# Optimization experiments

Measured on AMD Instinct MI355X. Metric: run time of the kernel, lower is better.

The kernel has to match this reference:

```python
import jax, jax.numpy as jnp
import numpy as np

K = 15  # dynamic kernel size (out conv emits 15*15=225 channels)


def conv3x3(x, w, b):
    # x: [B,C,H,W], w: [O,I,3,3] (OIHW), 'SAME' padding, stride 1
    y = jax.lax.conv_general_dilated(
        x, w, window_strides=(1, 1), padding='SAME',
        dimension_numbers=('NCHW', 'OIHW', 'NCHW'))
    return y + b[None, :, None, None]


def res_block(x, wa, ba, wb, bb):
    # ResidualBlock_noBN: x + conv(relu(conv(x)))
    return x + conv3x3(jax.nn.relu(conv3x3(x, wa, ba)), wb, bb)


def setup_inputs() -> dict:
    key = jax.random.key(0)
    ks = jax.random.split(key, 12)
    nf = 64

    def w(k, o, i):
        return jax.random.normal(k, (o, i, 3, 3), jnp.float32) * 0.05

    return {
        'data_with_est': jax.random.normal(ks[0], (4, 6, 256, 256), jnp.float32),
        'data': jax.random.normal(ks[1], (4, 3, 256, 256), jnp.float32),
        'w_first': w(ks[2], nf, 6), 'b_first': jnp.zeros((nf,), jnp.float32),
        'w1a': w(ks[3], nf, nf), 'b1a': jnp.zeros((nf,), jnp.float32),
        'w1b': w(ks[4], nf, nf), 'b1b': jnp.zeros((nf,), jnp.float32),
        'w2a': w(ks[5], nf, nf), 'b2a': jnp.zeros((nf,), jnp.float32),
        'w2b': w(ks[6], nf, nf), 'b2b': jnp.zeros((nf,), jnp.float32),
        'w3a': w(ks[7], nf, nf), 'b3a': jnp.zeros((nf,), jnp.float32),
        'w3b': w(ks[8], nf, nf), 'b3b': jnp.zeros((nf,), jnp.float32),
        'w_out': w(ks[9], K * K, nf), 'b_out': jnp.zeros((K * K,), jnp.float32),
    }


def kernel_conv(frames, core):
    # frames: [B,3,H,W]; core: [B,225,H,W]
    B, C, H, W = frames.shape
    # per-pixel softmax over the 225 kernel taps of |core| (N=1, color=1 in original view)
    weights = jax.nn.softmax(jnp.abs(core), axis=1)  # [B, K*K, H, W]
    p = K // 2
    pad = jnp.pad(frames, ((0, 0), (0, 0), (p, p), (p, p)))
    shifts = jnp.arange(K)

    def win(i, j):  # shifted window, matches frame_pad[..., i:i+H, j:j+W]
        return jax.lax.dynamic_slice(pad, (0, 0, i, j), (B, C, H, W))

    # [K, K, B, C, H, W]; flattened index i*K+j matches torch stacking order
    patches = jax.vmap(lambda i: jax.vmap(lambda j: win(i, j))(shifts))(shifts)
    patches = patches.reshape(K * K, B, C, H, W)
    pred = jnp.einsum('bkhw,kbchw->bchw', weights, patches)  # sum over taps
    return pred


def reference(data_with_est, data,
              w_first, b_first,
              w1a, b1a, w1b, b1b,
              w2a, b2a, w2b, b2b,
              w3a, b3a, w3b, b3b,
              w_out, b_out):
    x = conv3x3(data_with_est, w_first, b_first)
    x = res_block(x, w1a, b1a, w1b, b1b)
    x = res_block(x, w2a, b2a, w2b, b2b)
    x = res_block(x, w3a, b3a, w3b, b3b)
    core = conv3x3(x, w_out, b_out)  # [B,225,H,W]
    pred = kernel_conv(data, core)   # [B,3,H,W]
    # original returns [frames, pred]
    return (data, pred)
```

## Files before the change

kernel.cpp:

```cpp
#include <hip/hip_runtime.h>

#define HW 256
#define PW 258
#define PP (PW * PW)
#define NPIX (HW * HW)

using short8 = __attribute__((ext_vector_type(8))) short;
using short4v = __attribute__((ext_vector_type(4))) short;
using f32x4 = __attribute__((ext_vector_type(4))) float;
using h4 = __attribute__((ext_vector_type(4))) _Float16;
using h8 = __attribute__((ext_vector_type(8))) _Float16;

#define GLD_LDS(g, l)                                                  \
  __builtin_amdgcn_global_load_lds(                                    \
      (const __attribute__((address_space(1))) void*)(g),              \
      (__attribute__((address_space(3))) void*)(l), 16, 0, 0)

static __device__ __forceinline__ ushort f2bf(float f) {
  unsigned u = __float_as_uint(f);
  unsigned r = (u + 0x7FFFu + ((u >> 16) & 1u)) >> 16;
  return (ushort)r;
}
static __device__ __forceinline__ float bf2f(ushort u) {
  return __uint_as_float(((unsigned)u) << 16);
}

__global__ void pack_in_k(const float* __restrict__ din, ushort* __restrict__ xp) {
  int i = blockIdx.x * 256 + threadIdx.x;
  int b = i >> 16;
  int px = i & 65535;
  int y = px >> 8, x = px & 255;
  short8 v;
#pragma unroll
  for (int z = 0; z < 8; ++z) v[z] = 0;
#pragma unroll
  for (int ic = 0; ic < 6; ++ic)
    v[ic] = (short)f2bf(din[(b * 6 + ic) * NPIX + px]);
  *(short8*)&xp[((size_t)b * PP + (size_t)(y + 1) * PW + (x + 1)) * 8] = v;
}

__global__ void zero_halo_k(ushort* __restrict__ x, ushort* __restrict__ y,
                            ushort* __restrict__ xp) {
  int i = blockIdx.x * 256 + threadIdx.x;
  if (i >= 4 * 1028) return;
  int b = i / 1028;
  int h = i - b * 1028;
  int py, px;
  if (h < 258) { py = 0; px = h; }
  else if (h < 516) { py = 257; px = h - 258; }
  else if (h < 772) { py = h - 516 + 1; px = 0; }
  else { py = h - 772 + 1; px = 257; }
  size_t p = (size_t)b * PP + (size_t)py * PW + px;
  short8 z;
#pragma unroll
  for (int k = 0; k < 8; ++k) z[k] = 0;
#pragma unroll
  for (int c8 = 0; c8 < 8; ++c8) {
    *(short8*)&x[p * 64 + c8 * 8] = z;
    *(short8*)&y[p * 64 + c8 * 8] = z;
  }
  *(short8*)&xp[p * 8] = z;
}

__global__ void pack_wfrag_k(const float* __restrict__ w,
                             ushort* __restrict__ wf, int OC, int CIN,
                             int CPAD, int NG, int total) {
  int i = blockIdx.x * 256 + threadIdx.x;
  if (i >= total) return;
  int j = i & 7;
  int lane = (i >> 3) & 63;
  int rest = i >> 9;
  int g = rest % NG;
  int ks = rest / NG;
  int oc = g * 16 + (lane & 15);
  int k = ks * 32 + (lane >> 4) * 8 + j;
  int t = k / CPAD;
  int ic = k - t * CPAD;
  float v = 0.f;
  if (oc < OC && t < 9 && ic < CIN) v = w[(oc * CIN + ic) * 9 + t];
  wf[i] = f2bf(v);
}

template <int C, int KS, bool RELU, bool RESID>
__global__ __launch_bounds__(256, 2) void conv_mfma_k(
    const ushort* __restrict__ in, const ushort* __restrict__ wf,
    const float* __restrict__ bias, const ushort* __restrict__ resid,
    ushort* __restrict__ out) {
  constexpr int CV = C / 8;
  constexpr int SROW = 66 * CV;
  constexpr int TOT = 6 * SROW;
  constexpr int LSLOT = ((TOT + 63) / 64) * 64;
  constexpr int W = (KS > 6) ? 6 : KS;
  __shared__ __align__(16) ushort xs[LSLOT * 8];

  const int tid = threadIdx.x;
  const int wave = tid >> 6, lane = tid & 63;
  const int quad = lane >> 4, l15 = lane & 15;
  const int x0 = blockIdx.x * 64, y0 = blockIdx.y * 4, b = blockIdx.z;
  const ushort* inb = in + (size_t)b * PP * C;
  const ushort* wfl = wf + (size_t)lane * 8;

  for (int s0 = wave * 64; s0 < TOT; s0 += 256) {
    int s = s0 + lane;
    int row, col, chunk;
    if (C == 64) {
      row = s / SROW;
      int r = s - row * SROW;
      col = r >> 3;
      chunk = (r & 7) ^ (col & 7);
    } else {
      row = s / 66;
      col = s - row * 66;
      chunk = 0;
    }
    GLD_LDS(inb + ((size_t)(y0 + row) * PW + (x0 + col)) * C + chunk * 8,
            &xs[(size_t)s0 * 8]);
  }

  short8 Wa[4][W];
  auto loadA = [&](int slot, int ks) {
#pragma unroll
    for (int mt = 0; mt < 4; ++mt)
      Wa[mt][slot] = *(const short8*)&wfl[(size_t)(ks * 4 + mt) * 512];
  };
#pragma unroll
  for (int ks = 0; ks < W; ++ks) loadA(ks, ks);

  __syncthreads();

  f32x4 acc[4][4];
#pragma unroll
  for (int mt = 0; mt < 4; ++mt)
#pragma unroll
    for (int nt = 0; nt < 4; ++nt)
#pragma unroll
      for (int r = 0; r < 4; ++r) acc[mt][nt][r] = 0.f;

  auto loadB = [&](short8* B, int ks) {
    int t, chunk;
    if (C == 64) {
      t = ks >> 1;
      chunk = ((ks & 1) << 2) + quad;
    } else {
      t = ks * 4 + quad;
      if (t > 8) t = 8;
      chunk = 0;
    }
    int dy = t / 3, dx = t - (t / 3) * 3;
#pragma unroll
    for (int nt = 0; nt < 4; ++nt) {
      int c = nt * 16 + l15 + dx;
      int slot = (C == 64)
                     ? ((wave + dy) * SROW + c * 8 + (chunk ^ (c & 7)))
                     : ((wave + dy) * 66 + c);
      B[nt] = *(const short8*)&xs[(size_t)slot * 8];
    }
  };

  short8 B0[4], B1[4];
  loadB(B0, 0);
#pragma unroll
  for (int ks = 0; ks < KS; ++ks) {
    if (ks + 1 < KS) loadB(B1, ks + 1);
    const int slot = ks % W;
#pragma unroll
    for (int nt = 0; nt < 4; ++nt)
#pragma unroll
      for (int mt = 0; mt < 4; ++mt)
        acc[mt][nt] = __builtin_amdgcn_mfma_f32_16x16x32_bf16(
            Wa[mt][slot], B0[nt], acc[mt][nt], 0, 0, 0);
    if (ks + W < KS) loadA(slot, ks + W);
#pragma unroll
    for (int nt = 0; nt < 4; ++nt) B0[nt] = B1[nt];
  }

  const int yw = y0 + wave;
#pragma unroll
  for (int mt = 0; mt < 4; ++mt) {
    const float4 bb = *(const float4*)&bias[mt * 16 + quad * 4];
#pragma unroll
    for (int nt = 0; nt < 4; ++nt) {
      int px = x0 + nt * 16 + l15;
      size_t base = ((size_t)b * PP + (size_t)(yw + 1) * PW + (px + 1)) * 64 +
                    mt * 16 + quad * 4;
      float v0 = acc[mt][nt][0] + bb.x;
      float v1 = acc[mt][nt][1] + bb.y;
      float v2 = acc[mt][nt][2] + bb.z;
      float v3 = acc[mt][nt][3] + bb.w;
      if (RELU) {
        v0 = fmaxf(v0, 0.f); v1 = fmaxf(v1, 0.f);
        v2 = fmaxf(v2, 0.f); v3 = fmaxf(v3, 0.f);
      }
      if (RESID) {
        short4v rv = *(const short4v*)&resid[base];
        v0 += bf2f((ushort)rv[0]); v1 += bf2f((ushort)rv[1]);
        v2 += bf2f((ushort)rv[2]); v3 += bf2f((ushort)rv[3]);
      }
      short4v o;
      o[0] = (short)f2bf(v0); o[1] = (short)f2bf(v1);
      o[2] = (short)f2bf(v2); o[3] = (short)f2bf(v3);
      *(short4v*)&out[base] = o;
    }
  }
}

__global__ __launch_bounds__(256, 2) void out_kc_k(
    const ushort* __restrict__ x, const ushort* __restrict__ wf,
    const float* __restrict__ b_out, const float* __restrict__ data,
    float* __restrict__ pred) {
  __shared__ __align__(16) char uni[64 * 264 * 2];
  __shared__ float dsh[3][15][78];
  __shared__ float bsh[256];
  ushort* xs = (ushort*)uni;
  _Float16* coreSh = (_Float16*)uni;

  const int tid = threadIdx.x;
  const int wave = tid >> 6, lane = tid & 63;
  const int quad = lane >> 4, l15 = lane & 15;
  const int x0 = blockIdx.x * 64, y = blockIdx.y, b = blockIdx.z;
  const ushort* wfl = wf + (size_t)lane * 8;

  for (int s0 = wave * 64; s0 < 3 * 528; s0 += 256) {
    int s = s0 + lane;
    int row = s / 528;
    int r = s - row * 528;
    int col = r >> 3;
    int chunk = (r & 7) ^ (col & 7);
    const ushort* g = x + ((size_t)b * PP + (size_t)(y + row) * PW +
                           (x0 + col)) * 64 + chunk * 8;
    GLD_LDS(g, &xs[(size_t)s0 * 8]);
  }
  bsh[tid] = (tid < 225) ? b_out[tid] : 0.f;
  for (int i = tid; i < 3 * 15 * 78; i += 256) {
    int ch = i / 1170;
    int rem = i - ch * 1170;
    int r = rem / 78;
    int cc = rem - r * 78;
    int gy = y - 7 + r, gx = x0 - 7 + cc;
    float v = 0.f;
    if ((unsigned)gy < (unsigned)HW && (unsigned)gx < (unsigned)HW)
      v = data[((b * 3 + ch) << 16) + (gy << 8) + gx];
    dsh[ch][r][cc] = v;
  }

  short8 Wa[4][6];
  auto loadA = [&](int slot, int ks) {
#pragma unroll
    for (int mt = 0; mt < 4; ++mt)
      Wa[mt][slot] =
          *(const short8*)&wfl[(size_t)((ks * 16 + wave * 4 + mt)) * 512];
  };
#pragma unroll
  for (int ks = 0; ks < 6; ++ks) loadA(ks, ks);

  __syncthreads();

  f32x4 acc[4][4];
#pragma unroll
  for (int mt = 0; mt < 4; ++mt)
#pragma unroll
    for (int nt = 0; nt < 4; ++nt)
#pragma unroll
      for (int r = 0; r < 4; ++r) acc[mt][nt][r] = 0.f;

  auto loadB = [&](short8* B, int ks) {
    int t = ks >> 1;
    int dy = t / 3, dx = t - (t / 3) * 3;
    int chunk = ((ks & 1) << 2) + quad;
#pragma unroll
    for (int nt = 0; nt < 4; ++nt) {
      int c = nt * 16 + l15 + dx;
      int slot = dy * 528 + c * 8 + (chunk ^ (c & 7));
      B[nt] = *(const short8*)&xs[(size_t)slot * 8];
    }
  };

  short8 B0[4], B1[4];
  loadB(B0, 0);
#pragma unroll
  for (int ks = 0; ks < 18; ++ks) {
    if (ks + 1 < 18) loadB(B1, ks + 1);
    const int slot = ks % 6;
#pragma unroll
    for (int nt = 0; nt < 4; ++nt)
#pragma unroll
      for (int mt = 0; mt < 4; ++mt)
        acc[mt][nt] = __builtin_amdgcn_mfma_f32_16x16x32_bf16(
            Wa[mt][slot], B0[nt], acc[mt][nt], 0, 0, 0);
    if (ks + 6 < 18) loadA(slot, ks + 6);
#pragma unroll
    for (int nt = 0; nt < 4; ++nt) B0[nt] = B1[nt];
  }
  __syncthreads();

#pragma unroll
  for (int mt = 0; mt < 4; ++mt) {
    int c0 = wave * 64 + mt * 16 + quad * 4;
#pragma unroll
    for (int nt = 0; nt < 4; ++nt) {
      int px = nt * 16 + l15;
      h4 hv;
#pragma unroll
      for (int r = 0; r < 4; ++r) {
        int c = c0 + r;
        float a = acc[mt][nt][r] + bsh[c];
        a = (c < 225) ? fabsf(a) : -1e4f;
        hv[r] = (_Float16)a;
      }
      *(h4*)&coreSh[px * 264 + c0] = hv;
    }
  }
  __syncthreads();

  const int px = wave * 16 + l15;
  const int cbase = quad * 64;
  h8 vals[8];
#pragma unroll
  for (int v = 0; v < 8; ++v)
    vals[v] = *(h8*)&coreSh[px * 264 + cbase + v * 8];

  float m = 0.f;
#pragma unroll
  for (int v = 0; v < 8; ++v)
#pragma unroll
    for (int z = 0; z < 8; ++z) m = fmaxf(m, (float)vals[v][z]);
  m = fmaxf(m, __shfl_xor(m, 16));
  m = fmaxf(m, __shfl_xor(m, 32));

  float l = 0.f, p0 = 0.f, p1 = 0.f, p2 = 0.f;
#pragma unroll
  for (int v = 0; v < 8; ++v)
#pragma unroll
    for (int z = 0; z < 8; ++z) {
      int c = cbase + v * 8 + z;
      float a = (float)vals[v][z];
      float e = __expf(a - m);
      l += e;
      if (c < 225) {
        int di = (int)(((unsigned)c * 34953u) >> 19);
        int dj = c - di * 15;
        p0 += e * dsh[0][di][px + dj];
        p1 += e * dsh[1][di][px + dj];
        p2 += e * dsh[2][di][px + dj];
      }
    }
  l += __shfl_xor(l, 16);  l += __shfl_xor(l, 32);
  p0 += __shfl_xor(p0, 16); p0 += __shfl_xor(p0, 32);
  p1 += __shfl_xor(p1, 16); p1 += __shfl_xor(p1, 32);
  p2 += __shfl_xor(p2, 16); p2 += __shfl_xor(p2, 32);

  if (quad == 0) {
    float inv = 1.f / l;
    int pix = (y << 8) + x0 + px;
    pred[((b * 3 + 0) << 16) + pix] = p0 * inv;
    pred[((b * 3 + 1) << 16) + pix] = p1 * inv;
    pred[((b * 3 + 2) << 16) + pix] = p2 * inv;
  }
}

__global__ void copy_k(const float4* __restrict__ src, float4* __restrict__ dst,
                       int n4) {
  int i = blockIdx.x * blockDim.x + threadIdx.x;
  if (i < n4) dst[i] = src[i];
}

extern "C" void kernel_launch(void* const* d_in, const int* in_sizes, int n_in,
                              void* d_out, int out_size, void* d_ws,
                              size_t ws_size, hipStream_t stream) {
  const float* data_with_est = (const float*)d_in[0];
  const float* data = (const float*)d_in[1];
  const float* w_first = (const float*)d_in[2];
  const float* b_first = (const float*)d_in[3];
  const float* wa[3] = {(const float*)d_in[4], (const float*)d_in[8],
                        (const float*)d_in[12]};
  const float* ba[3] = {(const float*)d_in[5], (const float*)d_in[9],
                        (const float*)d_in[13]};
  const float* wb[3] = {(const float*)d_in[6], (const float*)d_in[10],
                        (const float*)d_in[14]};
  const float* bb[3] = {(const float*)d_in[7], (const float*)d_in[11],
                        (const float*)d_in[15]};
  const float* w_out = (const float*)d_in[16];
  const float* b_out = (const float*)d_in[17];

  float* out = (float*)d_out;
  float* pred = out + 4 * 3 * NPIX;

  ushort* x = (ushort*)d_ws;
  ushort* y = x + (size_t)4 * PP * 64;
  ushort* xp = y + (size_t)4 * PP * 64;
  ushort* Wp1 = xp + (size_t)4 * PP * 8;
  ushort* Wpr = Wp1 + 6144;
  ushort* Wpo = Wpr + 6 * 36864;

  pack_in_k<<<1024, 256, 0, stream>>>(data_with_est, xp);
  zero_halo_k<<<17, 256, 0, stream>>>(x, y, xp);
  pack_wfrag_k<<<24, 256, 0, stream>>>(w_first, Wp1, 64, 6, 8, 4, 6144);
  for (int i = 0; i < 3; ++i) {
    pack_wfrag_k<<<144, 256, 0, stream>>>(wa[i], Wpr + (2 * i) * 36864, 64, 64,
                                          64, 4, 36864);
    pack_wfrag_k<<<144, 256, 0, stream>>>(wb[i], Wpr + (2 * i + 1) * 36864, 64,
                                          64, 64, 4, 36864);
  }
  pack_wfrag_k<<<576, 256, 0, stream>>>(w_out, Wpo, 225, 64, 64, 16, 147456);

  dim3 cgrid(4, 64, 4), cblk(256);
  conv_mfma_k<8, 3, false, false>
      <<<cgrid, cblk, 0, stream>>>(xp, Wp1, b_first, nullptr, x);
  for (int i = 0; i < 3; ++i) {
    conv_mfma_k<64, 18, true, false><<<cgrid, cblk, 0, stream>>>(
        x, Wpr + (2 * i) * 36864, ba[i], nullptr, y);
    conv_mfma_k<64, 18, false, true><<<cgrid, cblk, 0, stream>>>(
        y, Wpr + (2 * i + 1) * 36864, bb[i], x, x);
  }
  out_kc_k<<<dim3(4, HW, 4), 256, 0, stream>>>(x, Wpo, b_out, data, pred);
  int n4 = 4 * 3 * NPIX / 4;
  copy_k<<<(n4 + 255) / 256, 256, 0, stream>>>((const float4*)data,
                                               (float4*)out, n4);
}
```

Before: 466.8 us.

## Merge prep launches, shrink weight prefetch ring, restructure softmax-kernel-conv epilogue

Combines input packing, halo zeroing and the output copy into one launch, and all weight-fragment packing into a second launch, cutting about ten small kernel launches. The weight register ring in the conv and output kernels shrinks from 6 to 4 slots, and the B double buffer now alternates by index instead of being copied, which reduces register pressure. The softmax/kernel-prediction epilogue now uses a transposed fp16 frame tile in LDS, so each lane handles whole kernel rows and reads vectorized h4 data instead of scalar float lookups per tap. Storing frame pixels in fp16 loses some precision, and the shorter prefetch distance may expose more weight-load latency.

```diff
diff --git a/kernel.cpp b/kernel.cpp
--- a/kernel.cpp
+++ b/kernel.cpp
@@ -9,7 +9,6 @@
 using short4v = __attribute__((ext_vector_type(4))) short;
 using f32x4 = __attribute__((ext_vector_type(4))) float;
 using h4 = __attribute__((ext_vector_type(4))) _Float16;
-using h8 = __attribute__((ext_vector_type(8))) _Float16;
 
 #define GLD_LDS(g, l)                                                  \
   __builtin_amdgcn_global_load_lds(                                    \
@@ -25,53 +24,65 @@
   return __uint_as_float(((unsigned)u) << 16);
 }
 
-__global__ void pack_in_k(const float* __restrict__ din, ushort* __restrict__ xp) {
-  int i = blockIdx.x * 256 + threadIdx.x;
-  int b = i >> 16;
-  int px = i & 65535;
-  int y = px >> 8, x = px & 255;
-  short8 v;
-#pragma unroll
-  for (int z = 0; z < 8; ++z) v[z] = 0;
-#pragma unroll
-  for (int ic = 0; ic < 6; ++ic)
-    v[ic] = (short)f2bf(din[(b * 6 + ic) * NPIX + px]);
-  *(short8*)&xp[((size_t)b * PP + (size_t)(y + 1) * PW + (x + 1)) * 8] = v;
-}
-
-__global__ void zero_halo_k(ushort* __restrict__ x, ushort* __restrict__ y,
-                            ushort* __restrict__ xp) {
-  int i = blockIdx.x * 256 + threadIdx.x;
-  if (i >= 4 * 1028) return;
-  int b = i / 1028;
-  int h = i - b * 1028;
-  int py, px;
-  if (h < 258) { py = 0; px = h; }
-  else if (h < 516) { py = 257; px = h - 258; }
-  else if (h < 772) { py = h - 516 + 1; px = 0; }
-  else { py = h - 772 + 1; px = 257; }
-  size_t p = (size_t)b * PP + (size_t)py * PW + px;
-  short8 z;
-#pragma unroll
-  for (int k = 0; k < 8; ++k) z[k] = 0;
-#pragma unroll
-  for (int c8 = 0; c8 < 8; ++c8) {
-    *(short8*)&x[p * 64 + c8 * 8] = z;
-    *(short8*)&y[p * 64 + c8 * 8] = z;
-  }
-  *(short8*)&xp[p * 8] = z;
-}
-
-__global__ void pack_wfrag_k(const float* __restrict__ w,
-                             ushort* __restrict__ wf, int OC, int CIN,
-                             int CPAD, int NG, int total) {
-  int i = blockIdx.x * 256 + threadIdx.x;
+__global__ void prep_pack_k(const float* __restrict__ din,
+                            ushort* __restrict__ xp, ushort* __restrict__ x,
+                            ushort* __restrict__ y,
+                            const float4* __restrict__ data4,
+                            float4* __restrict__ out4) {
+  int blk = blockIdx.x, tid = threadIdx.x;
+  if (blk < 1024) {
+    int i = blk * 256 + tid;
+    int b = i >> 16;
+    int px = i & 65535;
+    int yy = px >> 8, xx = px & 255;
+    short8 v;
+#pragma unroll
+    for (int z = 0; z < 8; ++z) v[z] = 0;
+#pragma unroll
+    for (int ic = 0; ic < 6; ++ic)
+      v[ic] = (short)f2bf(din[(b * 6 + ic) * NPIX + px]);
+    *(short8*)&xp[((size_t)b * PP + (size_t)(yy + 1) * PW + (xx + 1)) * 8] = v;
+  } else if (blk < 1041) {
+    int i = (blk - 1024) * 256 + tid;
+    if (i >= 4 * 1028) return;
+    int b = i / 1028;
+    int h = i - b * 1028;
+    int py, px;
+    if (h < 258) { py = 0; px = h; }
+    else if (h < 516) { py = 257; px = h - 258; }
+    else if (h < 772) { py = h - 516 + 1; px = 0; }
+    else { py = h - 772 + 1; px = 257; }
+    size_t p = (size_t)b * PP + (size_t)py * PW + px;
+    short8 z;
+#pragma unroll
+    for (int k = 0; k < 8; ++k) z[k] = 0;
+#pragma unroll
+    for (int c8 = 0; c8 < 8; ++c8) {
+      *(short8*)&x[p * 64 + c8 * 8] = z;
+      *(short8*)&y[p * 64 + c8 * 8] = z;
+    }
+    *(short8*)&xp[p * 8] = z;
+  } else {
+    int i = (blk - 1041) * 256 + tid;
+    if (i < 196608) out4[i] = data4[i];
+  }
+}
+
+struct W8 { const float* w[8]; };
+
+static __device__ __forceinline__ void pack_one(const float* __restrict__ w,
+                                                ushort* __restrict__ wf, int OC,
+                                                int CIN, int CPAD, int i,
+                                                int total) {
   if (i >= total) return;
   int j = i & 7;
   int lane = (i >> 3) & 63;
   int rest = i >> 9;
-  int g = rest % NG;
-  int ks = rest / NG;
+  int NG = total >> 9;
+  (void)NG;
+  int NGr = (OC > 64) ? 16 : 4;
+  int g = rest % NGr;
+  int ks = rest / NGr;
   int oc = g * 16 + (lane & 15);
   int k = ks * 32 + (lane >> 4) * 8 + j;
   int t = k / CPAD;
@@ -79,6 +90,20 @@
   float v = 0.f;
   if (oc < OC && t < 9 && ic < CIN) v = w[(oc * CIN + ic) * 9 + t];
   wf[i] = f2bf(v);
+}
+
+__global__ void prep_w_k(W8 ws, ushort* __restrict__ base) {
+  int blk = blockIdx.x, tid = threadIdx.x;
+  if (blk < 24) {
+    pack_one(ws.w[0], base, 64, 6, 8, blk * 256 + tid, 6144);
+  } else if (blk < 888) {
+    int seg = (blk - 24) / 144;
+    int i = ((blk - 24) - seg * 144) * 256 + tid;
+    pack_one(ws.w[1 + seg], base + 6144 + seg * 36864, 64, 64, 64, i, 36864);
+  } else {
+    int i = (blk - 888) * 256 + tid;
+    pack_one(ws.w[7], base + 227328, 225, 64, 64, i, 147456);
+  }
 }
 
 template <int C, int KS, bool RELU, bool RESID>
@@ -90,7 +115,7 @@
   constexpr int SROW = 66 * CV;
   constexpr int TOT = 6 * SROW;
   constexpr int LSLOT = ((TOT + 63) / 64) * 64;
-  constexpr int W = (KS > 6) ? 6 : KS;
+  constexpr int W = (KS > 4) ? 4 : KS;
   __shared__ __align__(16) ushort xs[LSLOT * 8];
 
   const int tid = threadIdx.x;
@@ -157,21 +182,19 @@
     }
   };
 
-  short8 B0[4], B1[4];
-  loadB(B0, 0);
+  short8 Bbuf[2][4];
+  loadB(Bbuf[0], 0);
 #pragma unroll
   for (int ks = 0; ks < KS; ++ks) {
-    if (ks + 1 < KS) loadB(B1, ks + 1);
+    if (ks + 1 < KS) loadB(Bbuf[(ks + 1) & 1], ks + 1);
     const int slot = ks % W;
 #pragma unroll
     for (int nt = 0; nt < 4; ++nt)
 #pragma unroll
       for (int mt = 0; mt < 4; ++mt)
         acc[mt][nt] = __builtin_amdgcn_mfma_f32_16x16x32_bf16(
-            Wa[mt][slot], B0[nt], acc[mt][nt], 0, 0, 0);
+            Wa[mt][slot], Bbuf[ks & 1][nt], acc[mt][nt], 0, 0, 0);
     if (ks + W < KS) loadA(slot, ks + W);
-#pragma unroll
-    for (int nt = 0; nt < 4; ++nt) B0[nt] = B1[nt];
   }
 
   const int yw = y0 + wave;
@@ -209,7 +232,7 @@
     const float* __restrict__ b_out, const float* __restrict__ data,
     float* __restrict__ pred) {
   __shared__ __align__(16) char uni[64 * 264 * 2];
-  __shared__ float dsh[3][15][78];
+  __shared__ __align__(16) _Float16 dshT[3 * 80 * 20];
   __shared__ float bsh[256];
   ushort* xs = (ushort*)uni;
   _Float16* coreSh = (_Float16*)uni;
@@ -231,19 +254,19 @@
     GLD_LDS(g, &xs[(size_t)s0 * 8]);
   }
   bsh[tid] = (tid < 225) ? b_out[tid] : 0.f;
-  for (int i = tid; i < 3 * 15 * 78; i += 256) {
-    int ch = i / 1170;
-    int rem = i - ch * 1170;
+  for (int i = tid; i < 3 * 16 * 78; i += 256) {
+    int ch = i / 1248;
+    int rem = i - ch * 1248;
     int r = rem / 78;
-    int cc = rem - r * 78;
-    int gy = y - 7 + r, gx = x0 - 7 + cc;
+    int col = rem - r * 78;
+    int gy = y - 7 + r, gx = x0 - 7 + col;
     float v = 0.f;
     if ((unsigned)gy < (unsigned)HW && (unsigned)gx < (unsigned)HW)
       v = data[((b * 3 + ch) << 16) + (gy << 8) + gx];
-    dsh[ch][r][cc] = v;
-  }
-
-  short8 Wa[4][6];
+    dshT[(ch * 80 + col) * 20 + r] = (_Float16)v;
+  }
+
+  short8 Wa[4][4];
   auto loadA = [&](int slot, int ks) {
 #pragma unroll
     for (int mt = 0; mt < 4; ++mt)
@@ -251,7 +274,7 @@
           *(const short8*)&wfl[(size_t)((ks * 16 + wave * 4 + mt)) * 512];
   };
 #pragma unroll
-  for (int ks = 0; ks < 6; ++ks) loadA(ks, ks);
+  for (int ks = 0; ks < 4; ++ks) loadA(ks, ks);
 
   __syncthreads();
 
@@ -275,21 +298,19 @@
     }
   };
 
-  short8 B0[4], B1[4];
-  loadB(B0, 0);
+  short8 Bbuf[2][4];
+  loadB(Bbuf[0], 0);
 #pragma unroll
   for (int ks = 0; ks < 18; ++ks) {
-    if (ks + 1 < 18) loadB(B1, ks + 1);
-    const int slot = ks % 6;
+    if (ks + 1 < 18) loadB(Bbuf[(ks + 1) & 1], ks + 1);
+    const int slot = ks % 4;
 #pragma unroll
     for (int nt = 0; nt < 4; ++nt)
 #pragma unroll
       for (int mt = 0; mt < 4; ++mt)
         acc[mt][nt] = __builtin_amdgcn_mfma_f32_16x16x32_bf16(
-            Wa[mt][slot], B0[nt], acc[mt][nt], 0, 0, 0);
-    if (ks + 6 < 18) loadA(slot, ks + 6);
-#pragma unroll
-    for (int nt = 0; nt < 4; ++nt) B0[nt] = B1[nt];
+            Wa[mt][slot], Bbuf[ks & 1][nt], acc[mt][nt], 0, 0, 0);
+    if (ks + 4 < 18) loadA(slot, ks + 4);
   }
   __syncthreads();
 
@@ -313,43 +334,51 @@
   __syncthreads();
 
   const int px = wave * 16 + l15;
-  const int cbase = quad * 64;
-  h8 vals[8];
-#pragma unroll
-  for (int v = 0; v < 8; ++v)
-    vals[v] = *(h8*)&coreSh[px * 264 + cbase + v * 8];
+  const int q = quad;
+  h4 vals4[15];
+#pragma unroll
+  for (int k = 0; k < 15; ++k)
+    vals4[k] = *(h4*)&coreSh[px * 264 + q * 60 + k * 4];
 
   float m = 0.f;
 #pragma unroll
-  for (int v = 0; v < 8; ++v)
-#pragma unroll
-    for (int z = 0; z < 8; ++z) m = fmaxf(m, (float)vals[v][z]);
+  for (int k = 0; k < 15; ++k)
+#pragma unroll
+    for (int z = 0; z < 4; ++z) m = fmaxf(m, (float)vals4[k][z]);
   m = fmaxf(m, __shfl_xor(m, 16));
   m = fmaxf(m, __shfl_xor(m, 32));
 
-  float l = 0.f, p0 = 0.f, p1 = 0.f, p2 = 0.f;
-#pragma unroll
-  for (int v = 0; v < 8; ++v)
-#pragma unroll
-    for (int z = 0; z < 8; ++z) {
-      int c = cbase + v * 8 + z;
-      float a = (float)vals[v][z];
-      float e = __expf(a - m);
-      l += e;
-      if (c < 225) {
-        int di = (int)(((unsigned)c * 34953u) >> 19);
-        int dj = c - di * 15;
-        p0 += e * dsh[0][di][px + dj];
-        p1 += e * dsh[1][di][px + dj];
-        p2 += e * dsh[2][di][px + dj];
-      }
-    }
+  float e[60];
+  float l = 0.f;
+#pragma unroll
+  for (int k = 0; k < 15; ++k)
+#pragma unroll
+    for (int z = 0; z < 4; ++z) {
+      float t = __expf((float)vals4[k][z] - m);
+      e[k * 4 + z] = t;
+      l += t;
+    }
+
+  float p0 = 0.f, p1 = 0.f, p2 = 0.f;
+#pragma unroll
+  for (int dj = 0; dj < 15; ++dj) {
+    h4 d0 = *(h4*)&dshT[(0 * 80 + px + dj) * 20 + 4 * q];
+    h4 d1 = *(h4*)&dshT[(1 * 80 + px + dj) * 20 + 4 * q];
+    h4 d2 = *(h4*)&dshT[(2 * 80 + px + dj) * 20 + 4 * q];
+#pragma unroll
+    for (int rr = 0; rr < 4; ++rr) {
+      float ev = e[rr * 15 + dj];
+      p0 += ev * (float)d0[rr];
+      p1 += ev * (float)d1[rr];
+      p2 += ev * (float)d2[rr];
+    }
+  }
   l += __shfl_xor(l, 16);  l += __shfl_xor(l, 32);
   p0 += __shfl_xor(p0, 16); p0 += __shfl_xor(p0, 32);
   p1 += __shfl_xor(p1, 16); p1 += __shfl_xor(p1, 32);
   p2 += __shfl_xor(p2, 16); p2 += __shfl_xor(p2, 32);
 
-  if (quad == 0) {
+  if (q == 0) {
     float inv = 1.f / l;
     int pix = (y << 8) + x0 + px;
     pred[((b * 3 + 0) << 16) + pix] = p0 * inv;
@@ -358,28 +387,16 @@
   }
 }
 
-__global__ void copy_k(const float4* __restrict__ src, float4* __restrict__ dst,
-                       int n4) {
-  int i = blockIdx.x * blockDim.x + threadIdx.x;
-  if (i < n4) dst[i] = src[i];
-}
-
 extern "C" void kernel_launch(void* const* d_in, const int* in_sizes, int n_in,
                               void* d_out, int out_size, void* d_ws,
                               size_t ws_size, hipStream_t stream) {
   const float* data_with_est = (const float*)d_in[0];
   const float* data = (const float*)d_in[1];
-  const float* w_first = (const float*)d_in[2];
   const float* b_first = (const float*)d_in[3];
-  const float* wa[3] = {(const float*)d_in[4], (const float*)d_in[8],
-                        (const float*)d_in[12]};
   const float* ba[3] = {(const float*)d_in[5], (const float*)d_in[9],
                         (const float*)d_in[13]};
-  const float* wb[3] = {(const float*)d_in[6], (const float*)d_in[10],
-                        (const float*)d_in[14]};
   const float* bb[3] = {(const float*)d_in[7], (const float*)d_in[11],
                         (const float*)d_in[15]};
-  const float* w_out = (const float*)d_in[16];
   const float* b_out = (const float*)d_in[17];
 
   float* out = (float*)d_out;
@@ -388,20 +405,20 @@
   ushort* x = (ushort*)d_ws;
   ushort* y = x + (size_t)4 * PP * 64;
   ushort* xp = y + (size_t)4 * PP * 64;
-  ushort* Wp1 = xp + (size_t)4 * PP * 8;
-  ushort* Wpr = Wp1 + 6144;
-  ushort* Wpo = Wpr + 6 * 36864;
-
-  pack_in_k<<<1024, 256, 0, stream>>>(data_with_est, xp);
-  zero_halo_k<<<17, 256, 0, stream>>>(x, y, xp);
-  pack_wfrag_k<<<24, 256, 0, stream>>>(w_first, Wp1, 64, 6, 8, 4, 6144);
-  for (int i = 0; i < 3; ++i) {
-    pack_wfrag_k<<<144, 256, 0, stream>>>(wa[i], Wpr + (2 * i) * 36864, 64, 64,
-                                          64, 4, 36864);
-    pack_wfrag_k<<<144, 256, 0, stream>>>(wb[i], Wpr + (2 * i + 1) * 36864, 64,
-                                          64, 64, 4, 36864);
-  }
-  pack_wfrag_k<<<576, 256, 0, stream>>>(w_out, Wpo, 225, 64, 64, 16, 147456);
+  ushort* Wb = xp + (size_t)4 * PP * 8;
+  ushort* Wp1 = Wb;
+  ushort* Wpr = Wb + 6144;
+  ushort* Wpo = Wb + 227328;
+
+  prep_pack_k<<<1809, 256, 0, stream>>>(data_with_est, xp, x, y,
+                                        (const float4*)data, (float4*)out);
+  W8 ws;
+  ws.w[0] = (const float*)d_in[2];
+  ws.w[1] = (const float*)d_in[4];  ws.w[2] = (const float*)d_in[6];
+  ws.w[3] = (const float*)d_in[8];  ws.w[4] = (const float*)d_in[10];
+  ws.w[5] = (const float*)d_in[12]; ws.w[6] = (const float*)d_in[14];
+  ws.w[7] = (const float*)d_in[16];
+  prep_w_k<<<1464, 256, 0, stream>>>(ws, Wb);
 
   dim3 cgrid(4, 64, 4), cblk(256);
   conv_mfma_k<8, 3, false, false>
@@ -413,7 +430,4 @@
         y, Wpr + (2 * i + 1) * 36864, bb[i], x, x);
   }
   out_kc_k<<<dim3(4, HW, 4), 256, 0, stream>>>(x, Wpo, b_out, data, pred);
-  int n4 = 4 * 3 * NPIX / 4;
-  copy_k<<<(n4 + 255) / 256, 256, 0, stream>>>((const float4*)data,
-                                               (float4*)out, n4);
-}
+}
```

Result: faster. 443.1 us (-5.1%).
